# Kernel tuning notes

Measured on AMD Instinct MI355X. Metric: run time of the kernel, lower is better.

Reference implementation:

```python
import jax, jax.numpy as jnp
import numpy as np

MAX_DISP = 4  # max_displacement; window = (2*MAX_DISP+1)**2 = 81 displacements


def setup_inputs() -> dict:
    key = jax.random.key(0)
    k1, k2 = jax.random.split(key)
    B, C, H, W = 8, 128, 128, 128
    in1 = jax.random.normal(k1, (B, C, H, W), dtype=jnp.float32)
    in2 = jax.random.normal(k2, (B, C, H, W), dtype=jnp.float32)
    return {"in1": in1, "in2": in2}


def reference(in1, in2):
    # Cost-volume correlation (kernel_size=1): for each displacement (dy,dx) in
    # [-d, d]^2, corr[b, w, y, x] = mean_c in1[b,c,y,x] * in2_pad[b,c,y+dy,x+dx],
    # matching torch unfold ordering: w = dy_idx*(2d+1) + dx_idx (row-major).
    B, C, H, W = in1.shape
    d = MAX_DISP
    in2_pad = jnp.pad(in2, ((0, 0), (0, 0), (d, d), (d, d)))  # zero pad, like ConstantPad2d
    corr = [
        jnp.mean(in1 * jax.lax.slice(in2_pad, (0, 0, dy, dx), (B, C, dy + H, dx + W)), axis=1)
        for dy in range(2 * d + 1)
        for dx in range(2 * d + 1)
    ]
    return jnp.stack(corr, axis=1)  # [B, (2d+1)^2, H, W]
```

## Files before the change

### kernel.cpp

```cpp
#include <hip/hip_runtime.h>


#define MAXD 4
#define ND 9
#define NDISP 81
#define BATCH 8
#define CH 128
#define HH 128
#define WW 128
#define CC 8
#define NCHUNK (CH / CC)
#define TY 4
#define NROW (TY + 2 * MAXD)
#define XW 64
#define P2 72
#define NT 576
#define NQ 18

__global__ __launch_bounds__(NT, 5) void corr_kernel(
    const float* __restrict__ in1,
    const float* __restrict__ in2,
    float* __restrict__ out)
{
    __shared__ float s2[NROW * CC * P2];

    const int tid   = threadIdx.x;
    const int b     = blockIdx.x;
    const int y0    = blockIdx.y * TY;
    const int xbase = blockIdx.z * XW;

    const int ly = tid / (ND * 16);
    const int dy = (tid / 16) % ND;
    const int xg = tid & 15;
    const int x0 = xg * 4;
    const int rl = ly + dy;

    float acc[ND][4];
    #pragma unroll
    for (int d = 0; d < ND; ++d)
        #pragma unroll
        for (int i = 0; i < 4; ++i) acc[d][i] = 0.0f;

    const float* in2b   = in2 + (size_t)b * CH * HH * WW;
    const float* in1row = in1 + (size_t)b * CH * HH * WW
                              + (size_t)(y0 + ly) * WW + xbase;

    for (int ch = 0; ch < NCHUNK; ++ch) {
        const int c0 = ch * CC;
        __syncthreads();

        #pragma unroll
        for (int jj = 0; jj < 3; ++jj) {
            int j   = tid + jj * NT;
            int row = j / (CC * NQ);
            int rem = j - row * (CC * NQ);
            int c   = rem / NQ;
            int q   = rem - c * NQ;
            int r   = y0 + row - MAXD;
            int gx  = xbase - MAXD + q * 4;
            float4 v = make_float4(0.0f, 0.0f, 0.0f, 0.0f);
            if (r >= 0 && r < HH && gx >= 0 && gx + 3 < WW)
                v = *(const float4*)(in2b + ((size_t)(c0 + c) * HH + r) * WW + gx);
            *(float4*)&s2[(row * CC + c) * P2 + q * 4] = v;
        }
        __syncthreads();

        #pragma unroll
        for (int c = 0; c < CC; ++c) {
            const float* p1 = in1row + (size_t)(c0 + c) * HH * WW;
            float4 a = *(const float4*)(p1 + x0);
            float aa[4] = {a.x, a.y, a.z, a.w};

            const float* s2r = &s2[(rl * CC + c) * P2 + x0];
            float4 b0 = *(const float4*)(s2r);
            float4 b1 = *(const float4*)(s2r + 4);
            float4 b2 = *(const float4*)(s2r + 8);
            float bb[12] = {b0.x, b0.y, b0.z, b0.w,
                            b1.x, b1.y, b1.z, b1.w,
                            b2.x, b2.y, b2.z, b2.w};

            #pragma unroll
            for (int d = 0; d < ND; ++d)
                #pragma unroll
                for (int i = 0; i < 4; ++i)
                    acc[d][i] = fmaf(aa[i], bb[i + d], acc[d][i]);
        }
    }

    const float scale = 1.0f / (float)CH;
    float* outb = out + (size_t)b * NDISP * HH * WW
                      + (size_t)(y0 + ly) * WW + xbase;
    #pragma unroll
    for (int d = 0; d < ND; ++d) {
        float* op = outb + (size_t)(dy * ND + d) * HH * WW;
        float4 v = make_float4(acc[d][0] * scale, acc[d][1] * scale,
                               acc[d][2] * scale, acc[d][3] * scale);
        *(float4*)(op + x0) = v;
    }
}

extern "C" void kernel_launch(void* const* d_in, const int* in_sizes, int n_in,
                              void* d_out, int out_size, void* d_ws, size_t ws_size,
                              hipStream_t stream) {
    const float* in1 = (const float*)d_in[0];
    const float* in2 = (const float*)d_in[1];
    float* out = (float*)d_out;
    dim3 grid(BATCH, HH / TY, WW / XW);
    corr_kernel<<<grid, NT, 0, stream>>>(in1, in2, out);
}
```

Measured before the change: 232.1 us.

## Drop shared-memory staging; load in2 directly with register double-buffering over channels

Removes the LDS tile and its per-chunk barriers. Each thread now reads its in1 and in2 rows straight from global memory, using a two-deep register prefetch across channels. Each thread covers 8 x-positions instead of 4, so the block spans the full width and the grid loses its z dimension. Zero padding is handled by redirecting out-of-range loads to a zeroed workspace buffer with stride 0, which a tiny extra kernel fills on every launch. In exchange, data reuse now depends on the L1/L2 caches, and the doubled accumulator array (72 floats) raises register pressure and may lower occupancy.

```diff
diff --git a/kernel.cpp b/kernel.cpp
--- a/kernel.cpp
+++ b/kernel.cpp
@@ -8,94 +8,118 @@
 #define CH 128
 #define HH 128
 #define WW 128
-#define CC 8
-#define NCHUNK (CH / CC)
 #define TY 4
-#define NROW (TY + 2 * MAXD)
-#define XW 64
-#define P2 72
 #define NT 576
-#define NQ 18
 
-__global__ __launch_bounds__(NT, 5) void corr_kernel(
+__global__ void zero_ws_kernel(float* ws) {
+    ws[threadIdx.x] = 0.0f;
+}
+
+__global__ __launch_bounds__(NT) void corr_kernel(
     const float* __restrict__ in1,
     const float* __restrict__ in2,
+    const float* __restrict__ zbuf,
     float* __restrict__ out)
 {
-    __shared__ float s2[NROW * CC * P2];
-
-    const int tid   = threadIdx.x;
-    const int b     = blockIdx.x;
-    const int y0    = blockIdx.y * TY;
-    const int xbase = blockIdx.z * XW;
+    const int tid = threadIdx.x;
+    const int b   = blockIdx.x;
+    const int y0  = blockIdx.y * TY;
 
     const int ly = tid / (ND * 16);
     const int dy = (tid / 16) % ND;
     const int xg = tid & 15;
-    const int x0 = xg * 4;
-    const int rl = ly + dy;
+    const int x0 = xg * 8;
+    const int y  = y0 + ly;
+    const int r  = y + dy - MAXD;
+    const bool rok  = (r >= 0) && (r < HH);
+    const bool q0ok = rok && (xg > 0);
+    const bool q3ok = rok && (xg < 15);
 
-    float acc[ND][4];
+    const int cs = HH * WW;
+
+    const float* p1   = in1 + ((size_t)b * CH) * cs + y * WW + x0;
+    const float* rowp = in2 + ((size_t)b * CH) * cs + (rok ? r : 0) * WW;
+    const float* pl = q0ok ? (rowp + x0 - 4) : zbuf;
+    const float* pm = rok  ? (rowp + x0)     : zbuf;
+    const float* ph = q3ok ? (rowp + x0 + 8) : zbuf;
+    const int sl = q0ok ? cs : 0;
+    const int sm = rok  ? cs : 0;
+    const int sh = q3ok ? cs : 0;
+
+    float acc[ND][8];
     #pragma unroll
     for (int d = 0; d < ND; ++d)
         #pragma unroll
-        for (int i = 0; i < 4; ++i) acc[d][i] = 0.0f;
+        for (int i = 0; i < 8; ++i) acc[d][i] = 0.0f;
 
-    const float* in2b   = in2 + (size_t)b * CH * HH * WW;
-    const float* in1row = in1 + (size_t)b * CH * HH * WW
-                              + (size_t)(y0 + ly) * WW + xbase;
+    auto do_fma = [&](const float4& Aa, const float4& Ab,
+                      const float4& Wl, const float4& Wm0,
+                      const float4& Wm1, const float4& Wh) {
+        float a[8]  = {Aa.x, Aa.y, Aa.z, Aa.w, Ab.x, Ab.y, Ab.z, Ab.w};
+        float w[16] = {Wl.x,  Wl.y,  Wl.z,  Wl.w,
+                       Wm0.x, Wm0.y, Wm0.z, Wm0.w,
+                       Wm1.x, Wm1.y, Wm1.z, Wm1.w,
+                       Wh.x,  Wh.y,  Wh.z,  Wh.w};
+        #pragma unroll
+        for (int d = 0; d < ND; ++d)
+            #pragma unroll
+            for (int i = 0; i < 8; ++i)
+                acc[d][i] = fmaf(a[i], w[i + d], acc[d][i]);
+    };
 
-    for (int ch = 0; ch < NCHUNK; ++ch) {
-        const int c0 = ch * CC;
-        __syncthreads();
+    float4 A0a, A0b, W0l, W0m0, W0m1, W0h;
+    float4 A1a, A1b, W1l, W1m0, W1m1, W1h;
 
-        #pragma unroll
-        for (int jj = 0; jj < 3; ++jj) {
-            int j   = tid + jj * NT;
-            int row = j / (CC * NQ);
-            int rem = j - row * (CC * NQ);
-            int c   = rem / NQ;
-            int q   = rem - c * NQ;
-            int r   = y0 + row - MAXD;
-            int gx  = xbase - MAXD + q * 4;
-            float4 v = make_float4(0.0f, 0.0f, 0.0f, 0.0f);
-            if (r >= 0 && r < HH && gx >= 0 && gx + 3 < WW)
-                v = *(const float4*)(in2b + ((size_t)(c0 + c) * HH + r) * WW + gx);
-            *(float4*)&s2[(row * CC + c) * P2 + q * 4] = v;
-        }
-        __syncthreads();
+    A0a  = *(const float4*)(p1);
+    A0b  = *(const float4*)(p1 + 4);
+    W0l  = *(const float4*)(pl);
+    W0m0 = *(const float4*)(pm);
+    W0m1 = *(const float4*)(pm + 4);
+    W0h  = *(const float4*)(ph);
 
-        #pragma unroll
-        for (int c = 0; c < CC; ++c) {
-            const float* p1 = in1row + (size_t)(c0 + c) * HH * WW;
-            float4 a = *(const float4*)(p1 + x0);
-            float aa[4] = {a.x, a.y, a.z, a.w};
+    #pragma unroll 1
+    for (int c = 0; c < CH - 2; c += 2) {
+        A1a  = *(const float4*)(p1 + cs);
+        A1b  = *(const float4*)(p1 + cs + 4);
+        W1l  = *(const float4*)(pl + sl);
+        W1m0 = *(const float4*)(pm + sm);
+        W1m1 = *(const float4*)(pm + sm + 4);
+        W1h  = *(const float4*)(ph + sh);
 
-            const float* s2r = &s2[(rl * CC + c) * P2 + x0];
-            float4 b0 = *(const float4*)(s2r);
-            float4 b1 = *(const float4*)(s2r + 4);
-            float4 b2 = *(const float4*)(s2r + 8);
-            float bb[12] = {b0.x, b0.y, b0.z, b0.w,
-                            b1.x, b1.y, b1.z, b1.w,
-                            b2.x, b2.y, b2.z, b2.w};
+        do_fma(A0a, A0b, W0l, W0m0, W0m1, W0h);
 
-            #pragma unroll
-            for (int d = 0; d < ND; ++d)
-                #pragma unroll
-                for (int i = 0; i < 4; ++i)
-                    acc[d][i] = fmaf(aa[i], bb[i + d], acc[d][i]);
-        }
+        p1 += 2 * cs;
+        pl += 2 * sl;  pm += 2 * sm;  ph += 2 * sh;
+        A0a  = *(const float4*)(p1);
+        A0b  = *(const float4*)(p1 + 4);
+        W0l  = *(const float4*)(pl);
+        W0m0 = *(const float4*)(pm);
+        W0m1 = *(const float4*)(pm + 4);
+        W0h  = *(const float4*)(ph);
+
+        do_fma(A1a, A1b, W1l, W1m0, W1m1, W1h);
     }
 
+    A1a  = *(const float4*)(p1 + cs);
+    A1b  = *(const float4*)(p1 + cs + 4);
+    W1l  = *(const float4*)(pl + sl);
+    W1m0 = *(const float4*)(pm + sm);
+    W1m1 = *(const float4*)(pm + sm + 4);
+    W1h  = *(const float4*)(ph + sh);
+    do_fma(A0a, A0b, W0l, W0m0, W0m1, W0h);
+    do_fma(A1a, A1b, W1l, W1m0, W1m1, W1h);
+
     const float scale = 1.0f / (float)CH;
-    float* outb = out + (size_t)b * NDISP * HH * WW
-                      + (size_t)(y0 + ly) * WW + xbase;
+    float* outb = out + (size_t)b * NDISP * cs + (size_t)y * WW + x0;
     #pragma unroll
     for (int d = 0; d < ND; ++d) {
-        float* op = outb + (size_t)(dy * ND + d) * HH * WW;
-        float4 v = make_float4(acc[d][0] * scale, acc[d][1] * scale,
-                               acc[d][2] * scale, acc[d][3] * scale);
-        *(float4*)(op + x0) = v;
+        float* op = outb + (size_t)(dy * ND + d) * cs;
+        float4 v0 = make_float4(acc[d][0] * scale, acc[d][1] * scale,
+                                acc[d][2] * scale, acc[d][3] * scale);
+        float4 v1 = make_float4(acc[d][4] * scale, acc[d][5] * scale,
+                                acc[d][6] * scale, acc[d][7] * scale);
+        *(float4*)(op)     = v0;
+        *(float4*)(op + 4) = v1;
     }
 }
 
@@ -105,6 +129,9 @@
     const float* in1 = (const float*)d_in[0];
     const float* in2 = (const float*)d_in[1];
     float* out = (float*)d_out;
-    dim3 grid(BATCH, HH / TY, WW / XW);
-    corr_kernel<<<grid, NT, 0, stream>>>(in1, in2, out);
+    float* zbuf = (float*)d_ws;
+
+    zero_ws_kernel<<<1, 64, 0, stream>>>(zbuf);
+    dim3 grid(BATCH, HH / TY);
+    corr_kernel<<<grid, NT, 0, stream>>>(in1, in2, zbuf, out);
 }
```

After: 220.5 us. 5.0% less time.

## Double-buffer in2 staging and cover full row width per block

Applied to the files above, without the earlier changes.

Each block now covers the full 128-wide row, so every thread computes 8 x-positions instead of 4 and the in2 halo is loaded once per row band instead of twice. The in2 shared-memory tile is double-buffered, with the next channel chunk prefetched into registers while the current one is computed, to overlap global loads with FMAs. The channel chunk shrinks from 8 to 4 and per-block offsets are precomputed. The cost is twice the accumulator registers, lower occupancy (launch bounds 2), and half as many blocks in the grid.

```diff
diff --git a/kernel.cpp b/kernel.cpp
--- a/kernel.cpp
+++ b/kernel.cpp
@@ -8,26 +8,26 @@
 #define CH 128
 #define HH 128
 #define WW 128
-#define CC 8
+#define HW (HH * WW)
+#define CC 4
 #define NCHUNK (CH / CC)
 #define TY 4
 #define NROW (TY + 2 * MAXD)
-#define XW 64
-#define P2 72
+#define PITCH 136
+#define NQ 34
+#define NSTG (CC * NROW * NQ)
 #define NT 576
-#define NQ 18
 
-__global__ __launch_bounds__(NT, 5) void corr_kernel(
+__global__ __launch_bounds__(NT, 2) void corr_kernel(
     const float* __restrict__ in1,
     const float* __restrict__ in2,
     float* __restrict__ out)
 {
-    __shared__ float s2[NROW * CC * P2];
+    __shared__ float s2[2][CC * NROW * PITCH];
 
-    const int tid   = threadIdx.x;
-    const int b     = blockIdx.x;
-    const int y0    = blockIdx.y * TY;
-    const int xbase = blockIdx.z * XW;
+    const int tid = threadIdx.x;
+    const int b   = blockIdx.x;
+    const int y0  = blockIdx.y * TY;
 
     const int ly = tid / (ND * 16);
     const int dy = (tid / 16) % ND;
@@ -35,67 +35,112 @@
     const int x0 = xg * 4;
     const int rl = ly + dy;
 
-    float acc[ND][4];
+    const float* in1b = in1 + (size_t)b * CH * HW;
+    const float* in2b = in2 + (size_t)b * CH * HW;
+
+    size_t goff[3]; int loff[3]; bool ok[3], wr[3];
+    #pragma unroll
+    for (int it = 0; it < 3; ++it) {
+        int j   = tid + it * NT;
+        wr[it]  = j < NSTG;
+        int jj  = wr[it] ? j : 0;
+        int c   = jj / (NROW * NQ);
+        int rem = jj - c * (NROW * NQ);
+        int row = rem / NQ;
+        int q   = rem - row * NQ;
+        int r   = y0 + row - MAXD;
+        int gx  = q * 4 - MAXD;
+        ok[it]  = wr[it] && (r >= 0) && (r < HH) && (gx >= 0) && (gx < WW);
+        goff[it] = ok[it] ? ((size_t)c * HW + (size_t)r * WW + gx) : 0;
+        loff[it] = (c * NROW + row) * PITCH + q * 4;
+    }
+
+    float acc[ND][8];
     #pragma unroll
     for (int d = 0; d < ND; ++d)
         #pragma unroll
-        for (int i = 0; i < 4; ++i) acc[d][i] = 0.0f;
+        for (int i = 0; i < 8; ++i) acc[d][i] = 0.0f;
 
-    const float* in2b   = in2 + (size_t)b * CH * HH * WW;
-    const float* in1row = in1 + (size_t)b * CH * HH * WW
-                              + (size_t)(y0 + ly) * WW + xbase;
+    const float4 z4 = make_float4(0.0f, 0.0f, 0.0f, 0.0f);
 
-    for (int ch = 0; ch < NCHUNK; ++ch) {
-        const int c0 = ch * CC;
-        __syncthreads();
+    float4 stv[3];
+    #pragma unroll
+    for (int it = 0; it < 3; ++it)
+        stv[it] = ok[it] ? *(const float4*)(in2b + goff[it]) : z4;
+    #pragma unroll
+    for (int it = 0; it < 3; ++it)
+        if (wr[it]) *(float4*)&s2[0][loff[it]] = stv[it];
+    __syncthreads();
 
-        #pragma unroll
-        for (int jj = 0; jj < 3; ++jj) {
-            int j   = tid + jj * NT;
-            int row = j / (CC * NQ);
-            int rem = j - row * (CC * NQ);
-            int c   = rem / NQ;
-            int q   = rem - c * NQ;
-            int r   = y0 + row - MAXD;
-            int gx  = xbase - MAXD + q * 4;
-            float4 v = make_float4(0.0f, 0.0f, 0.0f, 0.0f);
-            if (r >= 0 && r < HH && gx >= 0 && gx + 3 < WW)
-                v = *(const float4*)(in2b + ((size_t)(c0 + c) * HH + r) * WW + gx);
-            *(float4*)&s2[(row * CC + c) * P2 + q * 4] = v;
-        }
-        __syncthreads();
+    int p = 0;
+    #pragma unroll 1
+    for (int k = 0; k < NCHUNK; ++k) {
+        const int c0 = k * CC;
 
+        float4 aA[CC], aB[CC];
         #pragma unroll
         for (int c = 0; c < CC; ++c) {
-            const float* p1 = in1row + (size_t)(c0 + c) * HH * WW;
-            float4 a = *(const float4*)(p1 + x0);
-            float aa[4] = {a.x, a.y, a.z, a.w};
+            const float* p1 = in1b + (size_t)(c0 + c) * HW + (y0 + ly) * WW;
+            aA[c] = *(const float4*)(p1 + x0);
+            aB[c] = *(const float4*)(p1 + x0 + 64);
+        }
 
-            const float* s2r = &s2[(rl * CC + c) * P2 + x0];
-            float4 b0 = *(const float4*)(s2r);
-            float4 b1 = *(const float4*)(s2r + 4);
-            float4 b2 = *(const float4*)(s2r + 8);
-            float bb[12] = {b0.x, b0.y, b0.z, b0.w,
-                            b1.x, b1.y, b1.z, b1.w,
-                            b2.x, b2.y, b2.z, b2.w};
+        if (k + 1 < NCHUNK) {
+            const float* nb = in2b + (size_t)(k + 1) * CC * HW;
+            #pragma unroll
+            for (int it = 0; it < 3; ++it)
+                stv[it] = ok[it] ? *(const float4*)(nb + goff[it]) : z4;
+        }
+
+        const float* bufp = s2[p];
+        #pragma unroll
+        for (int c = 0; c < CC; ++c) {
+            const float* sr = bufp + (c * NROW + rl) * PITCH + x0;
+            float4 w0 = *(const float4*)(sr);
+            float4 w1 = *(const float4*)(sr + 4);
+            float4 w2 = *(const float4*)(sr + 8);
+            float4 w3 = *(const float4*)(sr + 64);
+            float4 w4 = *(const float4*)(sr + 68);
+            float4 w5 = *(const float4*)(sr + 72);
+            float wa[12] = {w0.x, w0.y, w0.z, w0.w,
+                            w1.x, w1.y, w1.z, w1.w,
+                            w2.x, w2.y, w2.z, w2.w};
+            float wb[12] = {w3.x, w3.y, w3.z, w3.w,
+                            w4.x, w4.y, w4.z, w4.w,
+                            w5.x, w5.y, w5.z, w5.w};
+            float a0[4] = {aA[c].x, aA[c].y, aA[c].z, aA[c].w};
+            float a1[4] = {aB[c].x, aB[c].y, aB[c].z, aB[c].w};
 
             #pragma unroll
             for (int d = 0; d < ND; ++d)
                 #pragma unroll
-                for (int i = 0; i < 4; ++i)
-                    acc[d][i] = fmaf(aa[i], bb[i + d], acc[d][i]);
+                for (int i = 0; i < 4; ++i) {
+                    acc[d][i]     = fmaf(a0[i], wa[i + d], acc[d][i]);
+                    acc[d][4 + i] = fmaf(a1[i], wb[i + d], acc[d][4 + i]);
+                }
         }
+        __syncthreads();
+
+        if (k + 1 < NCHUNK) {
+            #pragma unroll
+            for (int it = 0; it < 3; ++it)
+                if (wr[it]) *(float4*)&s2[1 - p][loff[it]] = stv[it];
+            p ^= 1;
+        }
+        __syncthreads();
     }
 
     const float scale = 1.0f / (float)CH;
-    float* outb = out + (size_t)b * NDISP * HH * WW
-                      + (size_t)(y0 + ly) * WW + xbase;
+    float* outb = out + (size_t)b * NDISP * HW + (size_t)(y0 + ly) * WW;
     #pragma unroll
     for (int d = 0; d < ND; ++d) {
-        float* op = outb + (size_t)(dy * ND + d) * HH * WW;
-        float4 v = make_float4(acc[d][0] * scale, acc[d][1] * scale,
-                               acc[d][2] * scale, acc[d][3] * scale);
-        *(float4*)(op + x0) = v;
+        float* op = outb + (size_t)(dy * ND + d) * HW;
+        float4 v0 = make_float4(acc[d][0] * scale, acc[d][1] * scale,
+                                acc[d][2] * scale, acc[d][3] * scale);
+        float4 v1 = make_float4(acc[d][4] * scale, acc[d][5] * scale,
+                                acc[d][6] * scale, acc[d][7] * scale);
+        *(float4*)(op + x0)      = v0;
+        *(float4*)(op + x0 + 64) = v1;
     }
 }
 
@@ -105,6 +150,6 @@
     const float* in1 = (const float*)d_in[0];
     const float* in2 = (const float*)d_in[1];
     float* out = (float*)d_out;
-    dim3 grid(BATCH, HH / TY, WW / XW);
+    dim3 grid(BATCH, HH / TY);
     corr_kernel<<<grid, NT, 0, stream>>>(in1, in2, out);
 }
```

After: 581.0 us. +150.4%, slower.
